# Performance work log

Hardware: AMD Instinct MI355X
Metric: run time of the kernel (lower is better)

## Reference

```python
import jax, jax.numpy as jnp
import numpy as np

B, S, D, H, E, K = 1, 2048, 1024, 16, 8, 2
DK = D // H          # 64 per-head key dim
FF = 4 * D           # 4096 expert hidden
EPS = 1e-5


def rmsnorm(x, scale):
    rms = jnp.sqrt(jnp.mean(x * x, axis=-1, keepdims=True) + EPS)
    return scale * (x / rms)


def setup_inputs() -> dict:
    key = jax.random.key(0)
    ks = jax.random.split(key, 12)
    std = 0.02
    x = jax.random.normal(ks[0], (B, S, D), dtype=jnp.float32)
    # causal mask: masked_fill where mask == 0
    self_attn_mask = jnp.tril(jnp.ones((S, S), dtype=jnp.int32))
    scale_attn = jnp.ones((D,), dtype=jnp.float32)
    scale_ffn = jnp.ones((D,), dtype=jnp.float32)
    # per-head projections, stacked: [H, DK, D] (torch Linear weight layout [out,in])
    Wq = jax.random.normal(ks[1], (H, DK, D), dtype=jnp.float32) * std
    Wk = jax.random.normal(ks[2], (H, DK, D), dtype=jnp.float32) * std
    Wv = jax.random.normal(ks[3], (H, DK, D), dtype=jnp.float32) * std
    Wo = jax.random.normal(ks[4], (D, D), dtype=jnp.float32) * std
    Wg = jax.random.normal(ks[5], (E, D), dtype=jnp.float32) * std   # router gate
    W_in = jax.random.normal(ks[6], (E, FF, D), dtype=jnp.float32) * std   # expert linear
    W_v = jax.random.normal(ks[7], (E, FF, D), dtype=jnp.float32) * std    # expert linear_v
    W_out = jax.random.normal(ks[8], (E, D, FF), dtype=jnp.float32) * std  # expert linear_out
    return {
        'x': x, 'self_attn_mask': self_attn_mask,
        'scale_attn': scale_attn, 'Wq': Wq, 'Wk': Wk, 'Wv': Wv, 'Wo': Wo,
        'scale_ffn': scale_ffn, 'Wg': Wg, 'W_in': W_in, 'W_v': W_v, 'W_out': W_out,
    }


def reference(x, self_attn_mask, scale_attn, Wq, Wk, Wv, Wo, scale_ffn, Wg, W_in, W_v, W_out):
    # --- self attention (pre-RMSNorm) ---
    normed = rmsnorm(x, scale_attn)
    q = jnp.einsum('bsd,hkd->bhsk', normed, Wq)
    k = jnp.einsum('bsd,hkd->bhsk', normed, Wk)
    v = jnp.einsum('bsd,hkd->bhsk', normed, Wv)
    attn = jnp.einsum('bhsk,bhtk->bhst', q, k) / np.sqrt(DK).astype(np.float32)
    attn = jnp.where(self_attn_mask[None, None] == 0, -jnp.inf, attn)
    attn = jax.nn.softmax(attn, axis=-1)
    ctx = jnp.einsum('bhst,bhtk->bhsk', attn, v)
    ctx = ctx.transpose(0, 2, 1, 3).reshape(x.shape[0], x.shape[1], D)  # concat heads
    a1 = ctx @ Wo.T
    x = x + a1
    # --- MoE (pre-RMSNorm) ---
    normed = rmsnorm(x, scale_ffn)
    router_logits = normed @ Wg.T                       # [B,S,E]
    router_probs = jax.nn.softmax(router_logits, axis=-1)
    gate, idx = jax.lax.top_k(router_probs, K)          # [B,S,K]
    gate = gate / jnp.sum(gate, axis=-1, keepdims=True)
    # combine weights per expert: sum of renormalized gates over selected slots
    onehot = (idx[..., None] == jnp.arange(E)).astype(x.dtype)  # [B,S,K,E]
    combine = jnp.sum(gate[..., None] * onehot, axis=2)         # [B,S,E]
    # all-expert dense FFN (faithful to the masked dense loop in torch)
    g = jax.nn.gelu(jnp.einsum('bsd,efd->bsef', normed, W_in), approximate=False)
    val = jnp.einsum('bsd,efd->bsef', normed, W_v)
    eo = jnp.einsum('bsef,edf->bsed', g * val, W_out)           # [B,S,E,D]
    moe_out = jnp.einsum('bse,bsed->bsd', combine, eo)
    out = x + moe_out
    return (out, router_probs)
```

## Files before the change

### kernel.cpp

```cpp
#include <hip/hip_runtime.h>
#include <hip/hip_bf16.h>
#include <math.h>

typedef unsigned int u32;
typedef unsigned short u16;
using bf16x8 = __attribute__((ext_vector_type(8))) short;
using f32x4 = __attribute__((ext_vector_type(4))) float;

#define MFMA_BF16(a, b, c) __builtin_amdgcn_mfma_f32_16x16x32_bf16((a), (b), (c), 0, 0, 0)
#define VMCNT8() asm volatile("s_waitcnt vmcnt(8)" ::: "memory")
#define VMCNT0() asm volatile("s_waitcnt vmcnt(0)" ::: "memory")
#define SBAR() __builtin_amdgcn_s_barrier()
#define SCHED0() __builtin_amdgcn_sched_barrier(0)

constexpr int kS = 2048, kD = 1024, kH = 16, kE = 8, kFF = 4096;
constexpr int kSlots = kS * 2;

__device__ __forceinline__ u16 bf16_rne(float f) {
  u32 u = __float_as_uint(f);
  u32 r = (u + 0x7fffu + ((u >> 16) & 1u)) >> 16;
  return (u16)r;
}
__device__ __forceinline__ float bf16_f32(u16 h) { return __uint_as_float(((u32)h) << 16); }
__device__ __forceinline__ u32 pack_hl(float x) {
  u16 hi = bf16_rne(x);
  u16 lo = bf16_rne(x - bf16_f32(hi));
  return ((u32)lo << 16) | (u32)hi;
}
__device__ __forceinline__ void unpack8(const u32* t, bf16x8& h, bf16x8& l) {
#pragma unroll
  for (int j = 0; j < 8; j++) {
    h[j] = (short)(t[j] & 0xffffu);
    l[j] = (short)(t[j] >> 16);
  }
}
__device__ __forceinline__ void gload_lds16(const void* g, void* l) {
  __builtin_amdgcn_global_load_lds((const __attribute__((address_space(1))) u32*)g,
                                   (__attribute__((address_space(3))) u32*)l, 16, 0, 0);
}

__global__ __launch_bounds__(256) void pack_dp3(const float* __restrict__ Wq,
                                                const float* __restrict__ Wk,
                                                const float* __restrict__ Wv,
                                                u16* __restrict__ o) {
  int i = blockIdx.x * 256 + threadIdx.x;
  if (i >= 3072 * 1024) return;
  int n = i >> 10, k = i & 1023;
  float v = (n < 1024) ? Wq[i] : (n < 2048) ? Wk[i - 1024 * 1024] : Wv[i - 2048 * 1024];
  u16 hi = bf16_rne(v);
  u16 lo = bf16_rne(v - bf16_f32(hi));
  size_t b = (size_t)n * 2048 + (size_t)(k >> 5) * 64 + (k & 31);
  o[b] = hi;
  o[b + 32] = lo;
}
__global__ __launch_bounds__(256) void pack_dp1(const float* __restrict__ W,
                                                u16* __restrict__ o, int n_elem) {
  int i = blockIdx.x * 256 + threadIdx.x;
  if (i >= n_elem) return;
  int k = i & 1023, n = i >> 10;
  float v = W[i];
  u16 hi = bf16_rne(v);
  u16 lo = bf16_rne(v - bf16_f32(hi));
  size_t b = (size_t)n * 2048 + (size_t)(k >> 5) * 64 + (k & 31);
  o[b] = hi;
  o[b + 32] = lo;
}
__global__ __launch_bounds__(256) void pack_bf16_kernel(const float* __restrict__ w,
                                                        u16* __restrict__ o, int n8) {
  int i = blockIdx.x * 256 + threadIdx.x;
  if (i >= n8) return;
  const float4* s = (const float4*)w + (size_t)i * 2;
  float4 a = s[0], b = s[1];
  u16 r[8] = {bf16_rne(a.x), bf16_rne(a.y), bf16_rne(a.z), bf16_rne(a.w),
              bf16_rne(b.x), bf16_rne(b.y), bf16_rne(b.z), bf16_rne(b.w)};
  *(uint4*)(o + (size_t)i * 8) = *(uint4*)r;
}

template <int MODE>
__global__ __launch_bounds__(256) void rmsnorm_kernel(
    const float* __restrict__ x, const float* __restrict__ scale,
    u16* __restrict__ odp, float* __restrict__ of32, u16* __restrict__ ob16) {
  const int s = blockIdx.x;
  const float* row = x + (size_t)s * kD;
  const int c = threadIdx.x * 4;
  float4 v = *(const float4*)(row + c);
  float ss = v.x * v.x + v.y * v.y + v.z * v.z + v.w * v.w;
#pragma unroll
  for (int m = 32; m; m >>= 1) ss += __shfl_xor(ss, m);
  __shared__ float wsum[4];
  if ((threadIdx.x & 63) == 0) wsum[threadIdx.x >> 6] = ss;
  __syncthreads();
  float tot = wsum[0] + wsum[1] + wsum[2] + wsum[3];
  float rinv = 1.0f / sqrtf(tot * (1.0f / kD) + 1e-5f);
  float4 sc = *(const float4*)(scale + c);
  float n[4] = {v.x * rinv * sc.x, v.y * rinv * sc.y, v.z * rinv * sc.z, v.w * rinv * sc.w};
  if (MODE == 0) {
    u16 hv[4], lv[4];
#pragma unroll
    for (int j = 0; j < 4; j++) {
      hv[j] = bf16_rne(n[j]);
      lv[j] = bf16_rne(n[j] - bf16_f32(hv[j]));
    }
    u16* o = odp + (size_t)s * 2048 + (size_t)(c >> 5) * 64 + (c & 31);
    *(uint2*)o = *(uint2*)hv;
    *(uint2*)(o + 32) = *(uint2*)lv;
  } else {
    *(float4*)(of32 + (size_t)s * kD + c) = make_float4(n[0], n[1], n[2], n[3]);
    u16* o = ob16 + (size_t)s * kD + c;
    o[0] = bf16_rne(n[0]); o[1] = bf16_rne(n[1]); o[2] = bf16_rne(n[2]); o[3] = bf16_rne(n[3]);
  }
}

template <int APK, int OUT>
__global__ __launch_bounds__(256) void gemm_dp(
    const void* __restrict__ Av, const u16* __restrict__ Bdp,
    const float* __restrict__ resid, int K,
    u32* __restrict__ oq, u32* __restrict__ ok, u32* __restrict__ ov,
    float* __restrict__ of) {
  __shared__ u16 As[2][128 * 64];
  __shared__ u16 Bs[2][128 * 64];
  const int tid = threadIdx.x, w = tid >> 6, l = tid & 63;
  const int m0 = blockIdx.y * 128, n0 = blockIdx.x * 128;
  const int wr = (w >> 1) * 64, wc = (w & 1) * 64;
  const char* Ab = (const char*)Av;
  const char* Bb = (const char*)Bdp;
  const size_t rowb = (size_t)K * 4;

  size_t asrc[4], bsrc[4];
  int dst[4];
#pragma unroll
  for (int i = 0; i < 4; i++) {
    int fl = i * 256 + tid;
    int row = fl >> 3, cb = fl & 7;
    size_t coff = (size_t)((cb ^ (row & 7)) * 16);
    asrc[i] = (size_t)(m0 + row) * rowb + coff;
    bsrc[i] = (size_t)(n0 + row) * rowb + coff;
    dst[i] = fl * 16;
  }

  f32x4 zero = {0.f, 0.f, 0.f, 0.f};
  f32x4 acc[4][4];
#pragma unroll
  for (int i = 0; i < 4; i++)
#pragma unroll
    for (int j = 0; j < 4; j++) acc[i][j] = zero;

  auto stage = [&](int buf, int s) {
    const char* ap = Ab + (size_t)s * 128;
    const char* bp = Bb + (size_t)s * 128;
#pragma unroll
    for (int i = 0; i < 4; i++) {
      gload_lds16(ap + asrc[i], (char*)&As[buf][0] + dst[i]);
      gload_lds16(bp + bsrc[i], (char*)&Bs[buf][0] + dst[i]);
    }
  };

  const int NS = K / 32;
  stage(0, 0);
  for (int s = 0; s < NS; s++) {
    const int cur = s & 1;
    const bool lastit = (s == NS - 1);
    if (!lastit) stage(cur ^ 1, s + 1);
    if (!lastit) VMCNT8(); else VMCNT0();
    SBAR();
    SCHED0();
    bf16x8 ah[4], al[4], bh[4], bl[4];
    const int g = l >> 4;
    if (APK) {
      const u32* At = (const u32*)&As[cur][0];
#pragma unroll
      for (int mi = 0; mi < 4; mi++) {
        int row = wr + mi * 16 + (l & 15);
        u32 t[8];
        *(uint4*)t = *(const uint4*)&At[row * 32 + (((2 * g) ^ (row & 7)) * 4)];
        *(uint4*)(t + 4) = *(const uint4*)&At[row * 32 + (((2 * g + 1) ^ (row & 7)) * 4)];
        unpack8(t, ah[mi], al[mi]);
      }
    } else {
#pragma unroll
      for (int mi = 0; mi < 4; mi++) {
        int row = wr + mi * 16 + (l & 15);
        ah[mi] = *(const bf16x8*)&As[cur][row * 64 + ((g ^ (row & 7)) * 8)];
        al[mi] = *(const bf16x8*)&As[cur][row * 64 + (((4 + g) ^ (row & 7)) * 8)];
      }
    }
#pragma unroll
    for (int ni = 0; ni < 4; ni++) {
      int row = wc + ni * 16 + (l & 15);
      bh[ni] = *(const bf16x8*)&Bs[cur][row * 64 + ((g ^ (row & 7)) * 8)];
      bl[ni] = *(const bf16x8*)&Bs[cur][row * 64 + (((4 + g) ^ (row & 7)) * 8)];
    }
#pragma unroll
    for (int mi = 0; mi < 4; mi++)
#pragma unroll
      for (int ni = 0; ni < 4; ni++) {
        f32x4 c = acc[mi][ni];
        c = MFMA_BF16(al[mi], bl[ni], c);
        c = MFMA_BF16(al[mi], bh[ni], c);
        c = MFMA_BF16(ah[mi], bl[ni], c);
        c = MFMA_BF16(ah[mi], bh[ni], c);
        acc[mi][ni] = c;
      }
    SCHED0();
    if (!lastit) SBAR();
  }

  if (OUT == 0) {
    u32* dstp;
    int nb;
    if (n0 < 1024) { dstp = oq; nb = n0; }
    else if (n0 < 2048) { dstp = ok; nb = n0 - 1024; }
    else { dstp = ov; nb = n0 - 2048; }
#pragma unroll
    for (int mi = 0; mi < 4; mi++)
#pragma unroll
      for (int ni = 0; ni < 4; ni++)
#pragma unroll
        for (int r = 0; r < 4; r++) {
          int row = m0 + wr + mi * 16 + ((l >> 4) << 2) + r;
          int col = nb + wc + ni * 16 + (l & 15);
          dstp[(size_t)row * 1024 + col] = pack_hl(acc[mi][ni][r]);
        }
  } else {
#pragma unroll
    for (int mi = 0; mi < 4; mi++)
#pragma unroll
      for (int ni = 0; ni < 4; ni++)
#pragma unroll
        for (int r = 0; r < 4; r++) {
          int row = m0 + wr + mi * 16 + ((l >> 4) << 2) + r;
          int col = n0 + wc + ni * 16 + (l & 15);
          of[(size_t)row * 1024 + col] = resid[(size_t)row * 1024 + col] + acc[mi][ni][r];
        }
  }
}

__global__ __launch_bounds__(256) void attn_kernel(
    const u32* __restrict__ Qp, const u32* __restrict__ Kp, const u32* __restrict__ Vp,
    u32* __restrict__ Op) {
  constexpr int LDK = 68;
  __shared__ u32 Ks[64 * LDK];
  __shared__ u32 Vs[64 * LDK];
  __shared__ u32 Ps[64 * LDK];
  const int tid = threadIdx.x, w = tid >> 6, l = tid & 63;
  const int qt = blockIdx.x, hh = blockIdx.y;
  const int q0 = qt * 64, hc = hh * 64;

  bf16x8 qh[2], ql[2];
  {
    const int qrow = q0 + w * 16 + (l & 15);
#pragma unroll
    for (int kk = 0; kk < 2; kk++) {
      u32 t[8];
      const u32* p = Qp + (size_t)qrow * kD + hc + kk * 32 + ((l >> 4) << 3);
      *(uint4*)t = *(const uint4*)p;
      *(uint4*)(t + 4) = *(const uint4*)(p + 4);
      unpack8(t, qh[kk], ql[kk]);
    }
  }
  float mrun[4], lrun[4];
  f32x4 zero = {0.f, 0.f, 0.f, 0.f};
  f32x4 oacc[4];
#pragma unroll
  for (int r = 0; r < 4; r++) { mrun[r] = -3.0e38f; lrun[r] = 0.f; }
#pragma unroll
  for (int vb = 0; vb < 4; vb++) oacc[vb] = zero;

  for (int kt = 0; kt <= qt; kt++) {
    __syncthreads();
    {
      const int trow = tid >> 2, c0 = (tid & 3) * 16;
      const u32* gK = Kp + (size_t)(kt * 64 + trow) * kD + hc + c0;
      u32* sK = Ks + trow * LDK + c0;
      *(uint4*)sK = *(const uint4*)gK;
      *(uint4*)(sK + 4) = *(const uint4*)(gK + 4);
      *(uint4*)(sK + 8) = *(const uint4*)(gK + 8);
      *(uint4*)(sK + 12) = *(const uint4*)(gK + 12);
      const u32* gV = Vp + (size_t)(kt * 64 + trow) * kD + hc + c0;
#pragma unroll
      for (int j = 0; j < 16; j += 4) {
        uint4 v = *(const uint4*)(gV + j);
        Vs[(c0 + j + 0) * LDK + trow] = v.x;
        Vs[(c0 + j + 1) * LDK + trow] = v.y;
        Vs[(c0 + j + 2) * LDK + trow] = v.z;
        Vs[(c0 + j + 3) * LDK + trow] = v.w;
      }
    }
    __syncthreads();

    f32x4 sfr[4];
#pragma unroll
    for (int kb = 0; kb < 4; kb++) {
      f32x4 sa = zero;
#pragma unroll
      for (int kk = 0; kk < 2; kk++) {
        u32 t[8];
        bf16x8 kh, kl;
        const u32* p = Ks + (kb * 16 + (l & 15)) * LDK + kk * 32 + ((l >> 4) << 3);
        *(uint4*)t = *(const uint4*)p;
        *(uint4*)(t + 4) = *(const uint4*)(p + 4);
        unpack8(t, kh, kl);
        sa = MFMA_BF16(ql[kk], kl, sa);
        sa = MFMA_BF16(ql[kk], kh, sa);
        sa = MFMA_BF16(qh[kk], kl, sa);
        sa = MFMA_BF16(qh[kk], kh, sa);
      }
      sfr[kb] = sa * 0.125f;
    }
    if (kt == qt) {
#pragma unroll
      for (int kb = 0; kb < 4; kb++) {
        int t = kt * 64 + kb * 16 + (l & 15);
#pragma unroll
        for (int r = 0; r < 4; r++) {
          int qq = q0 + w * 16 + ((l >> 4) << 2) + r;
          if (t > qq) sfr[kb][r] = -3.0e38f;
        }
      }
    }
#pragma unroll
    for (int r = 0; r < 4; r++) {
      float mx = fmaxf(fmaxf(sfr[0][r], sfr[1][r]), fmaxf(sfr[2][r], sfr[3][r]));
#pragma unroll
      for (int mm = 1; mm < 16; mm <<= 1) mx = fmaxf(mx, __shfl_xor(mx, mm));
      float mnew = fmaxf(mrun[r], mx);
      float sf = __expf(mrun[r] - mnew);
      mrun[r] = mnew;
      float rs = 0.f;
#pragma unroll
      for (int kb = 0; kb < 4; kb++) {
        float p = __expf(sfr[kb][r] - mnew);
        sfr[kb][r] = p;
        rs += p;
      }
#pragma unroll
      for (int mm = 1; mm < 16; mm <<= 1) rs += __shfl_xor(rs, mm);
      lrun[r] = lrun[r] * sf + rs;
#pragma unroll
      for (int vb = 0; vb < 4; vb++) oacc[vb][r] *= sf;
    }
#pragma unroll
    for (int kb = 0; kb < 4; kb++)
#pragma unroll
      for (int r = 0; r < 4; r++)
        Ps[(w * 16 + ((l >> 4) << 2) + r) * LDK + kb * 16 + (l & 15)] = pack_hl(sfr[kb][r]);
#pragma unroll
    for (int ks = 0; ks < 2; ks++) {
      bf16x8 ph, pl;
      {
        u32 t[8];
        const u32* pp = Ps + (w * 16 + (l & 15)) * LDK + ks * 32 + ((l >> 4) << 3);
        *(uint4*)t = *(const uint4*)pp;
        *(uint4*)(t + 4) = *(const uint4*)(pp + 4);
        unpack8(t, ph, pl);
      }
#pragma unroll
      for (int vb = 0; vb < 4; vb++) {
        u32 t2[8];
        bf16x8 vh, vl;
        const u32* pv = Vs + (vb * 16 + (l & 15)) * LDK + ks * 32 + ((l >> 4) << 3);
        *(uint4*)t2 = *(const uint4*)pv;
        *(uint4*)(t2 + 4) = *(const uint4*)(pv + 4);
        unpack8(t2, vh, vl);
        f32x4 c = oacc[vb];
        c = MFMA_BF16(pl, vl, c);
        c = MFMA_BF16(pl, vh, c);
        c = MFMA_BF16(ph, vl, c);
        c = MFMA_BF16(ph, vh, c);
        oacc[vb] = c;
      }
    }
  }
#pragma unroll
  for (int vb = 0; vb < 4; vb++)
#pragma unroll
    for (int r = 0; r < 4; r++) {
      float o = oacc[vb][r] / lrun[r];
      int row = q0 + w * 16 + ((l >> 4) << 2) + r;
      int col = hc + vb * 16 + (l & 15);
      Op[(size_t)row * kD + col] = pack_hl(o);
    }
}

__global__ __launch_bounds__(256) void router_kernel(
    const float* __restrict__ normed, const float* __restrict__ Wg,
    float* __restrict__ probs, float* __restrict__ gates,
    int* __restrict__ experts, int* __restrict__ counts) {
  const int w = threadIdx.x >> 6, l = threadIdx.x & 63;
  const int s = blockIdx.x * 4 + w;
  float lg[kE];
  const float* row = normed + (size_t)s * kD;
#pragma unroll
  for (int e = 0; e < kE; e++) {
    const float* wg = Wg + (size_t)e * kD;
    float a = 0.f;
    for (int d = l; d < kD; d += 64) a += row[d] * wg[d];
#pragma unroll
    for (int m = 32; m; m >>= 1) a += __shfl_xor(a, m);
    lg[e] = a;
  }
  if (l == 0) {
    float mx = lg[0];
#pragma unroll
    for (int e = 1; e < kE; e++) mx = fmaxf(mx, lg[e]);
    float p[kE], sum = 0.f;
#pragma unroll
    for (int e = 0; e < kE; e++) { p[e] = __expf(lg[e] - mx); sum += p[e]; }
    float inv = 1.f / sum;
#pragma unroll
    for (int e = 0; e < kE; e++) { p[e] *= inv; probs[(size_t)s * kE + e] = p[e]; }
    int i1 = 0;
#pragma unroll
    for (int e = 1; e < kE; e++) if (lg[e] > lg[i1]) i1 = e;
    int i2 = (i1 == 0) ? 1 : 0;
#pragma unroll
    for (int e = 0; e < kE; e++) if (e != i1 && lg[e] > lg[i2]) i2 = e;
    float den = 1.f / (p[i1] + p[i2]);
    gates[s * 2] = p[i1] * den;
    gates[s * 2 + 1] = p[i2] * den;
    experts[s * 2] = i1;
    experts[s * 2 + 1] = i2;
    atomicAdd(&counts[i1], 1);
    atomicAdd(&counts[i2], 1);
  }
}

__global__ void moe_init(int* counts) {
  if (threadIdx.x < kE) counts[threadIdx.x] = 0;
}
__global__ void moe_scan(const int* __restrict__ counts, int* __restrict__ ebase,
                         int* __restrict__ cursor) {
  if (threadIdx.x == 0) {
    int acc = 0;
    for (int e = 0; e < kE; e++) { ebase[e] = acc; cursor[e] = acc; acc += counts[e]; }
    ebase[kE] = acc;
  }
}
__global__ void moe_fill(const int* __restrict__ experts, int* __restrict__ cursor,
                         int* __restrict__ slot_list, int* __restrict__ slot_of) {
  int s = blockIdx.x * 256 + threadIdx.x;
  if (s >= kS) return;
  for (int k = 0; k < 2; k++) {
    int e = experts[s * 2 + k];
    int pos = atomicAdd(&cursor[e], 1);
    slot_list[pos] = s;
    slot_of[s * 2 + k] = pos;
  }
}

__global__ __launch_bounds__(512) void moe_mm1(
    const u16* __restrict__ A, const u16* __restrict__ B1g, const u16* __restrict__ B2g,
    const int* __restrict__ slot_list, const int* __restrict__ ebase,
    u16* __restrict__ Uo) {
  const int e = blockIdx.z;
  const int base = ebase[e];
  const int Me = ebase[e + 1] - base;
  const int m0 = blockIdx.y * 256;
  if (m0 >= Me) return;
  const int n0 = blockIdx.x * 128;
  __shared__ u16 As[2][256 * 64];
  __shared__ u16 B1s[2][128 * 64];
  __shared__ u16 B2s[2][128 * 64];
  const int tid = threadIdx.x, w = tid >> 6, l = tid & 63;
  const int wr = (w >> 2) * 128, wc = (w & 3) * 32;
  const char* B1 = (const char*)(B1g + (size_t)e * kFF * kD);
  const char* B2 = (const char*)(B2g + (size_t)e * kFF * kD);

  size_t asrc[4], bsrc[2];
  int adst[4], bdst[2];
#pragma unroll
  for (int i = 0; i < 4; i++) {
    int fl = i * 512 + tid;
    int row = fl >> 3, cb = fl & 7;
    int mr = m0 + row;
    if (mr > Me - 1) mr = Me - 1;
    int ar = slot_list[base + mr];
    asrc[i] = (size_t)ar * 2048 + (size_t)((cb ^ (row & 7)) * 16);
    adst[i] = fl * 16;
  }
#pragma unroll
  for (int i = 0; i < 2; i++) {
    int fl = i * 512 + tid;
    int row = fl >> 3, cb = fl & 7;
    bsrc[i] = (size_t)(n0 + row) * 2048 + (size_t)((cb ^ (row & 7)) * 16);
    bdst[i] = fl * 16;
  }

  f32x4 zero = {0.f, 0.f, 0.f, 0.f};
  f32x4 acc1[8][2], acc2[8][2];
#pragma unroll
  for (int i = 0; i < 8; i++)
#pragma unroll
    for (int j = 0; j < 2; j++) { acc1[i][j] = zero; acc2[i][j] = zero; }

  auto stage = [&](int buf, int s) {
    const size_t so = (size_t)s * 128;
    const char* ab = (const char*)A + so;
#pragma unroll
    for (int i = 0; i < 4; i++) gload_lds16(ab + asrc[i], (char*)&As[buf][0] + adst[i]);
#pragma unroll
    for (int i = 0; i < 2; i++) {
      gload_lds16(B1 + so + bsrc[i], (char*)&B1s[buf][0] + bdst[i]);
      gload_lds16(B2 + so + bsrc[i], (char*)&B2s[buf][0] + bdst[i]);
    }
  };

  const int NS = kD / 64;
  stage(0, 0);
  for (int s = 0; s < NS; s++) {
    const int cur = s & 1;
    const bool lastit = (s == NS - 1);
    if (!lastit) stage(cur ^ 1, s + 1);
    if (!lastit) VMCNT8(); else VMCNT0();
    SBAR();
    SCHED0();
#pragma unroll
    for (int kk = 0; kk < 2; kk++) {
      const int g = kk * 4 + (l >> 4);
      bf16x8 af[8], b1f[2], b2f[2];
#pragma unroll
      for (int mi = 0; mi < 8; mi++) {
        int row = wr + mi * 16 + (l & 15);
        af[mi] = *(const bf16x8*)&As[cur][row * 64 + ((g ^ (row & 7)) * 8)];
      }
#pragma unroll
      for (int ni = 0; ni < 2; ni++) {
        int row = wc + ni * 16 + (l & 15);
        int bo = row * 64 + ((g ^ (row & 7)) * 8);
        b1f[ni] = *(const bf16x8*)&B1s[cur][bo];
        b2f[ni] = *(const bf16x8*)&B2s[cur][bo];
      }
#pragma unroll
      for (int mi = 0; mi < 8; mi++)
#pragma unroll
        for (int ni = 0; ni < 2; ni++) {
          acc1[mi][ni] = MFMA_BF16(af[mi], b1f[ni], acc1[mi][ni]);
          acc2[mi][ni] = MFMA_BF16(af[mi], b2f[ni], acc2[mi][ni]);
        }
    }
    SCHED0();
    if (!lastit) SBAR();
  }

#pragma unroll
  for (int mi = 0; mi < 8; mi++)
#pragma unroll
    for (int r = 0; r < 4; r++) {
      int ml = m0 + wr + mi * 16 + ((l >> 4) << 2) + r;
      if (ml >= Me) continue;
      size_t rb = (size_t)(base + ml) * kFF;
#pragma unroll
      for (int ni = 0; ni < 2; ni++) {
        int col = n0 + wc + ni * 16 + (l & 15);
        float u = acc1[mi][ni][r], v2 = acc2[mi][ni][r];
        float ge = 0.5f * u * (1.0f + erff(u * 0.70710678118654752f));
        Uo[rb + col] = bf16_rne(ge * v2);
      }
    }
}

__global__ __launch_bounds__(256) void moe_mm2(
    const u16* __restrict__ U, const u16* __restrict__ Bg,
    const int* __restrict__ ebase, float* __restrict__ eo) {
  const int e = blockIdx.z;
  const int base = ebase[e];
  const int Me = ebase[e + 1] - base;
  const int m0 = blockIdx.y * 128;
  if (m0 >= Me) return;
  const int n0 = blockIdx.x * 128;
  __shared__ u16 As[2][128 * 64];
  __shared__ u16 Bs[2][128 * 64];
  const int tid = threadIdx.x, w = tid >> 6, l = tid & 63;
  const int wr = (w >> 1) * 64, wc = (w & 1) * 64;
  const char* B = (const char*)(Bg + (size_t)e * kD * kFF);

  size_t asrc[4], bsrc[4];
  int dst[4];
#pragma unroll
  for (int i = 0; i < 4; i++) {
    int fl = i * 256 + tid;
    int row = fl >> 3, cb = fl & 7;
    size_t coff = (size_t)((cb ^ (row & 7)) * 16);
    int mr = m0 + row;
    if (mr > Me - 1) mr = Me - 1;
    asrc[i] = (size_t)(base + mr) * 8192 + coff;
    bsrc[i] = (size_t)(n0 + row) * 8192 + coff;
    dst[i] = fl * 16;
  }

  f32x4 zero = {0.f, 0.f, 0.f, 0.f};
  f32x4 acc[4][4];
#pragma unroll
  for (int i = 0; i < 4; i++)
#pragma unroll
    for (int j = 0; j < 4; j++) acc[i][j] = zero;

  auto stage = [&](int buf, int s) {
    const size_t so = (size_t)s * 128;
#pragma unroll
    for (int i = 0; i < 4; i++) {
      gload_lds16((const char*)U + so + asrc[i], (char*)&As[buf][0] + dst[i]);
      gload_lds16(B + so + bsrc[i], (char*)&Bs[buf][0] + dst[i]);
    }
  };

  const int NS = kFF / 64;
  stage(0, 0);
  for (int s = 0; s < NS; s++) {
    const int cur = s & 1;
    const bool lastit = (s == NS - 1);
    if (!lastit) stage(cur ^ 1, s + 1);
    if (!lastit) VMCNT8(); else VMCNT0();
    SBAR();
    SCHED0();
#pragma unroll
    for (int kk = 0; kk < 2; kk++) {
      const int g = kk * 4 + (l >> 4);
      bf16x8 af[4], bf[4];
#pragma unroll
      for (int mi = 0; mi < 4; mi++) {
        int row = wr + mi * 16 + (l & 15);
        af[mi] = *(const bf16x8*)&As[cur][row * 64 + ((g ^ (row & 7)) * 8)];
      }
#pragma unroll
      for (int ni = 0; ni < 4; ni++) {
        int row = wc + ni * 16 + (l & 15);
        bf[ni] = *(const bf16x8*)&Bs[cur][row * 64 + ((g ^ (row & 7)) * 8)];
      }
#pragma unroll
      for (int mi = 0; mi < 4; mi++)
#pragma unroll
        for (int ni = 0; ni < 4; ni++) acc[mi][ni] = MFMA_BF16(af[mi], bf[ni], acc[mi][ni]);
    }
    SCHED0();
    if (!lastit) SBAR();
  }

#pragma unroll
  for (int mi = 0; mi < 4; mi++)
#pragma unroll
    for (int r = 0; r < 4; r++) {
      int ml = m0 + wr + mi * 16 + ((l >> 4) << 2) + r;
      if (ml >= Me) continue;
      size_t rb = (size_t)(base + ml) * kD;
#pragma unroll
      for (int ni = 0; ni < 4; ni++) {
        int col = n0 + wc + ni * 16 + (l & 15);
        eo[rb + col] = acc[mi][ni][r];
      }
    }
}

__global__ __launch_bounds__(256) void combine_kernel(
    const float* __restrict__ h, const float* __restrict__ eo,
    const float* __restrict__ gates, const int* __restrict__ slot_of,
    float* __restrict__ out) {
  const int s = blockIdx.x;
  const float g0 = gates[s * 2], g1 = gates[s * 2 + 1];
  const int p0 = slot_of[s * 2], p1 = slot_of[s * 2 + 1];
  const int c = threadIdx.x * 4;
  float4 hv = *(const float4*)(h + (size_t)s * kD + c);
  float4 e0 = *(const float4*)(eo + (size_t)p0 * kD + c);
  float4 e1 = *(const float4*)(eo + (size_t)p1 * kD + c);
  float4 o;
  o.x = hv.x + g0 * e0.x + g1 * e1.x;
  o.y = hv.y + g0 * e0.y + g1 * e1.y;
  o.z = hv.z + g0 * e0.z + g1 * e1.z;
  o.w = hv.w + g0 * e0.w + g1 * e1.w;
  *(float4*)(out + (size_t)s * kD + c) = o;
}

extern "C" void kernel_launch(void* const* d_in, const int* in_sizes, int n_in,
                              void* d_out, int out_size, void* d_ws, size_t ws_size,
                              hipStream_t stream) {
  (void)in_sizes; (void)n_in; (void)out_size; (void)ws_size;
  const float* x = (const float*)d_in[0];
  const float* scale_attn = (const float*)d_in[2];
  const float* Wq = (const float*)d_in[3];
  const float* Wk = (const float*)d_in[4];
  const float* Wv = (const float*)d_in[5];
  const float* Wo = (const float*)d_in[6];
  const float* scale_ffn = (const float*)d_in[7];
  const float* Wg = (const float*)d_in[8];
  const float* W_in = (const float*)d_in[9];
  const float* W_vv = (const float*)d_in[10];
  const float* W_out = (const float*)d_in[11];
  float* out = (float*)d_out;
  float* probs = out + (size_t)kS * kD;

  char* wsb = (char*)d_ws;
  size_t off = 0;
  auto alloc = [&](size_t bytes) -> void* {
    void* p = wsb + off;
    off += (bytes + 255) & ~(size_t)255;
    return p;
  };
  const size_t SDu = (size_t)kS * kD;
  const size_t EW = (size_t)kE * kFF * kD;
  u16* normA_dp = (u16*)alloc(SDu * 2 * 2);
  u32* qpk = (u32*)alloc(SDu * 4);
  u32* kpk = (u32*)alloc(SDu * 4);
  u32* vpk = (u32*)alloc(SDu * 4);
  u32* ctxpk = (u32*)alloc(SDu * 4);
  float* h = (float*)alloc(SDu * 4);
  float* normFf = (float*)alloc(SDu * 4);
  u16* normFb = (u16*)alloc(SDu * 2);
  u16* Wqkv_dp = (u16*)alloc((size_t)3072 * 2048 * 2);
  u16* Wo_dp = (u16*)alloc((size_t)1024 * 2048 * 2);
  u16* Win_bf = (u16*)alloc(EW * 2);
  u16* Wv_bf = (u16*)alloc(EW * 2);
  u16* Wout_bf = (u16*)alloc(EW * 2);
  u16* U = (u16*)alloc((size_t)kSlots * kFF * 2);
  float* eo = (float*)alloc((size_t)kSlots * kD * 4);
  float* gates = (float*)alloc(kS * 2 * 4);
  int* experts = (int*)alloc(kS * 2 * 4);
  int* slot_of = (int*)alloc(kS * 2 * 4);
  int* slot_list = (int*)alloc(kSlots * 4);
  int* counts = (int*)alloc(64);
  int* ebase = (int*)alloc(64);
  int* cursor = (int*)alloc(64);

  pack_dp3<<<(3072 * 1024) / 256, 256, 0, stream>>>(Wq, Wk, Wv, Wqkv_dp);
  pack_dp1<<<(1024 * 1024) / 256, 256, 0, stream>>>(Wo, Wo_dp, 1024 * 1024);
  const int n8 = (int)(EW / 8);
  pack_bf16_kernel<<<(n8 + 255) / 256, 256, 0, stream>>>(W_in, Win_bf, n8);
  pack_bf16_kernel<<<(n8 + 255) / 256, 256, 0, stream>>>(W_vv, Wv_bf, n8);
  pack_bf16_kernel<<<(n8 + 255) / 256, 256, 0, stream>>>(W_out, Wout_bf, n8);

  rmsnorm_kernel<0><<<kS, 256, 0, stream>>>(x, scale_attn, normA_dp, nullptr, nullptr);
  gemm_dp<0, 0><<<dim3(3072 / 128, kS / 128), 256, 0, stream>>>(
      normA_dp, Wqkv_dp, nullptr, kD, qpk, kpk, vpk, nullptr);
  attn_kernel<<<dim3(kS / 64, kH), 256, 0, stream>>>(qpk, kpk, vpk, ctxpk);
  gemm_dp<1, 1><<<dim3(1024 / 128, kS / 128), 256, 0, stream>>>(
      ctxpk, Wo_dp, x, kD, nullptr, nullptr, nullptr, h);

  rmsnorm_kernel<1><<<kS, 256, 0, stream>>>(h, scale_ffn, nullptr, normFf, normFb);
  moe_init<<<1, 64, 0, stream>>>(counts);
  router_kernel<<<kS / 4, 256, 0, stream>>>(normFf, Wg, probs, gates, experts, counts);
  moe_scan<<<1, 64, 0, stream>>>(counts, ebase, cursor);
  moe_fill<<<kS / 256, 256, 0, stream>>>(experts, cursor, slot_list, slot_of);

  moe_mm1<<<dim3(kFF / 128, kSlots / 256, kE), 512, 0, stream>>>(
      normFb, Win_bf, Wv_bf, slot_list, ebase, U);
  moe_mm2<<<dim3(kD / 128, kSlots / 128, kE), 256, 0, stream>>>(
      U, Wout_bf, ebase, eo);

  combine_kernel<<<kS, 256, 0, stream>>>(h, eo, gates, slot_of, out);
}
```

Measured before the change: 699.2 us.

## Use compacted tile map for MoE GEMMs, split GELU, prefetch attention K/V

The MoE GEMMs now launch over a compacted list of 128-row tiles built in moe_scan, so no blocks are spent on empty per-expert grid slots. W_in and W_v are packed into one concatenated matrix and computed by a single GEMM; a separate gelu_mul kernel then applies GELU and the gate product. moe_mm2 narrows its N tile to 64. The attention kernel register-prefetches the next K/V tile while the current one is computed. This adds a kernel launch and an extra round trip of the raw Uraw intermediate through memory, and Uraw is placed at the start of the workspace, where it aliases other buffers.

```diff
diff --git a/kernel.cpp b/kernel.cpp
--- a/kernel.cpp
+++ b/kernel.cpp
@@ -9,12 +9,14 @@
 
 #define MFMA_BF16(a, b, c) __builtin_amdgcn_mfma_f32_16x16x32_bf16((a), (b), (c), 0, 0, 0)
 #define VMCNT8() asm volatile("s_waitcnt vmcnt(8)" ::: "memory")
+#define VMCNT6() asm volatile("s_waitcnt vmcnt(6)" ::: "memory")
 #define VMCNT0() asm volatile("s_waitcnt vmcnt(0)" ::: "memory")
 #define SBAR() __builtin_amdgcn_s_barrier()
 #define SCHED0() __builtin_amdgcn_sched_barrier(0)
 
 constexpr int kS = 2048, kD = 1024, kH = 16, kE = 8, kFF = 4096;
-constexpr int kSlots = kS * 2;
+constexpr int kSlotCap = 5120;
+constexpr int kMaxTiles = 40;
 
 __device__ __forceinline__ u16 bf16_rne(float f) {
   u32 u = __float_as_uint(f);
@@ -64,6 +66,23 @@
   size_t b = (size_t)n * 2048 + (size_t)(k >> 5) * 64 + (k & 31);
   o[b] = hi;
   o[b + 32] = lo;
+}
+__global__ __launch_bounds__(256) void pack_winv(const float* __restrict__ Wi,
+                                                 const float* __restrict__ Wv,
+                                                 u16* __restrict__ o) {
+  size_t i8 = (size_t)blockIdx.x * 256 + threadIdx.x;
+  if (i8 >= (size_t)kE * 8192 * 1024 / 8) return;
+  size_t flat = i8 * 8;
+  int e = (int)(flat >> 23);
+  int r = (int)(flat & ((1u << 23) - 1));
+  int n = r >> 10, k = r & 1023;
+  const float* src = (n < 4096) ? Wi + ((size_t)e * 4096 + n) * 1024 + k
+                                : Wv + ((size_t)e * 4096 + (n - 4096)) * 1024 + k;
+  float4 a = *(const float4*)src;
+  float4 b = *(const float4*)(src + 4);
+  u16 rr[8] = {bf16_rne(a.x), bf16_rne(a.y), bf16_rne(a.z), bf16_rne(a.w),
+               bf16_rne(b.x), bf16_rne(b.y), bf16_rne(b.z), bf16_rne(b.w)};
+  *(uint4*)(o + flat) = *(uint4*)rr;
 }
 __global__ __launch_bounds__(256) void pack_bf16_kernel(const float* __restrict__ w,
                                                         u16* __restrict__ o, int n8) {
@@ -266,27 +285,41 @@
 #pragma unroll
   for (int vb = 0; vb < 4; vb++) oacc[vb] = zero;
 
+  const int trow = tid >> 2, c0v = (tid & 3) * 16;
+  const u32* gKb = Kp + hc + c0v;
+  const u32* gVb = Vp + hc + c0v;
+  uint4 kr[4], vr[4];
+  {
+    const u32* gK = gKb + (size_t)trow * kD;
+    kr[0] = *(const uint4*)gK; kr[1] = *(const uint4*)(gK + 4);
+    kr[2] = *(const uint4*)(gK + 8); kr[3] = *(const uint4*)(gK + 12);
+    const u32* gV = gVb + (size_t)trow * kD;
+    vr[0] = *(const uint4*)gV; vr[1] = *(const uint4*)(gV + 4);
+    vr[2] = *(const uint4*)(gV + 8); vr[3] = *(const uint4*)(gV + 12);
+  }
+
   for (int kt = 0; kt <= qt; kt++) {
+    {
+      u32* sK = Ks + trow * LDK + c0v;
+      *(uint4*)sK = kr[0]; *(uint4*)(sK + 4) = kr[1];
+      *(uint4*)(sK + 8) = kr[2]; *(uint4*)(sK + 12) = kr[3];
+#pragma unroll
+      for (int j = 0; j < 4; j++) {
+        Vs[(c0v + j * 4 + 0) * LDK + trow] = vr[j].x;
+        Vs[(c0v + j * 4 + 1) * LDK + trow] = vr[j].y;
+        Vs[(c0v + j * 4 + 2) * LDK + trow] = vr[j].z;
+        Vs[(c0v + j * 4 + 3) * LDK + trow] = vr[j].w;
+      }
+    }
     __syncthreads();
-    {
-      const int trow = tid >> 2, c0 = (tid & 3) * 16;
-      const u32* gK = Kp + (size_t)(kt * 64 + trow) * kD + hc + c0;
-      u32* sK = Ks + trow * LDK + c0;
-      *(uint4*)sK = *(const uint4*)gK;
-      *(uint4*)(sK + 4) = *(const uint4*)(gK + 4);
-      *(uint4*)(sK + 8) = *(const uint4*)(gK + 8);
-      *(uint4*)(sK + 12) = *(const uint4*)(gK + 12);
-      const u32* gV = Vp + (size_t)(kt * 64 + trow) * kD + hc + c0;
-#pragma unroll
-      for (int j = 0; j < 16; j += 4) {
-        uint4 v = *(const uint4*)(gV + j);
-        Vs[(c0 + j + 0) * LDK + trow] = v.x;
-        Vs[(c0 + j + 1) * LDK + trow] = v.y;
-        Vs[(c0 + j + 2) * LDK + trow] = v.z;
-        Vs[(c0 + j + 3) * LDK + trow] = v.w;
-      }
-    }
-    __syncthreads();
+    if (kt < qt) {
+      const u32* gK = gKb + (size_t)((kt + 1) * 64 + trow) * kD;
+      kr[0] = *(const uint4*)gK; kr[1] = *(const uint4*)(gK + 4);
+      kr[2] = *(const uint4*)(gK + 8); kr[3] = *(const uint4*)(gK + 12);
+      const u32* gV = gVb + (size_t)((kt + 1) * 64 + trow) * kD;
+      vr[0] = *(const uint4*)gV; vr[1] = *(const uint4*)(gV + 4);
+      vr[2] = *(const uint4*)(gV + 8); vr[3] = *(const uint4*)(gV + 12);
+    }
 
     f32x4 sfr[4];
 #pragma unroll
@@ -370,6 +403,7 @@
         oacc[vb] = c;
       }
     }
+    __syncthreads();
   }
 #pragma unroll
   for (int vb = 0; vb < 4; vb++)
@@ -429,11 +463,18 @@
   if (threadIdx.x < kE) counts[threadIdx.x] = 0;
 }
 __global__ void moe_scan(const int* __restrict__ counts, int* __restrict__ ebase,
-                         int* __restrict__ cursor) {
+                         int* __restrict__ cursor, int2* __restrict__ tmap) {
   if (threadIdx.x == 0) {
-    int acc = 0;
-    for (int e = 0; e < kE; e++) { ebase[e] = acc; cursor[e] = acc; acc += counts[e]; }
+    int acc = 0, t = 0;
+    for (int e = 0; e < kE; e++) {
+      ebase[e] = acc;
+      cursor[e] = acc;
+      int nt = (counts[e] + 127) >> 7;
+      for (int i = 0; i < nt; i++) tmap[t++] = make_int2(e, i * 128);
+      acc += nt << 7;
+    }
     ebase[kE] = acc;
+    for (; t < kMaxTiles; t++) tmap[t] = make_int2(-1, 0);
   }
 }
 __global__ void moe_fill(const int* __restrict__ experts, int* __restrict__ cursor,
@@ -448,60 +489,51 @@
   }
 }
 
-__global__ __launch_bounds__(512) void moe_mm1(
-    const u16* __restrict__ A, const u16* __restrict__ B1g, const u16* __restrict__ B2g,
-    const int* __restrict__ slot_list, const int* __restrict__ ebase,
-    u16* __restrict__ Uo) {
-  const int e = blockIdx.z;
-  const int base = ebase[e];
-  const int Me = ebase[e + 1] - base;
-  const int m0 = blockIdx.y * 256;
-  if (m0 >= Me) return;
+__global__ __launch_bounds__(256) void moe_mmA(
+    const u16* __restrict__ A, const u16* __restrict__ Bg,
+    const int* __restrict__ slot_list, const int* __restrict__ counts,
+    const int* __restrict__ ebase, const int2* __restrict__ tmap,
+    u16* __restrict__ Uraw) {
+  int2 tm = tmap[blockIdx.y];
+  const int e = tm.x;
+  if (e < 0) return;
+  const int base = ebase[e], Me = counts[e], m0 = tm.y;
   const int n0 = blockIdx.x * 128;
-  __shared__ u16 As[2][256 * 64];
-  __shared__ u16 B1s[2][128 * 64];
-  __shared__ u16 B2s[2][128 * 64];
+  __shared__ u16 As[2][128 * 64];
+  __shared__ u16 Bs[2][128 * 64];
   const int tid = threadIdx.x, w = tid >> 6, l = tid & 63;
-  const int wr = (w >> 2) * 128, wc = (w & 3) * 32;
-  const char* B1 = (const char*)(B1g + (size_t)e * kFF * kD);
-  const char* B2 = (const char*)(B2g + (size_t)e * kFF * kD);
-
-  size_t asrc[4], bsrc[2];
-  int adst[4], bdst[2];
+  const int wr = (w >> 1) * 64, wc = (w & 1) * 64;
+  const char* Ab = (const char*)A;
+  const char* Bb = (const char*)(Bg + ((size_t)e * 8192) * 1024);
+
+  size_t asrc[4], bsrc[4];
+  int dst[4];
 #pragma unroll
   for (int i = 0; i < 4; i++) {
-    int fl = i * 512 + tid;
+    int fl = i * 256 + tid;
     int row = fl >> 3, cb = fl & 7;
+    size_t coff = (size_t)((cb ^ (row & 7)) * 16);
     int mr = m0 + row;
     if (mr > Me - 1) mr = Me - 1;
     int ar = slot_list[base + mr];
-    asrc[i] = (size_t)ar * 2048 + (size_t)((cb ^ (row & 7)) * 16);
-    adst[i] = fl * 16;
-  }
-#pragma unroll
-  for (int i = 0; i < 2; i++) {
-    int fl = i * 512 + tid;
-    int row = fl >> 3, cb = fl & 7;
-    bsrc[i] = (size_t)(n0 + row) * 2048 + (size_t)((cb ^ (row & 7)) * 16);
-    bdst[i] = fl * 16;
+    asrc[i] = (size_t)ar * 2048 + coff;
+    bsrc[i] = (size_t)(n0 + row) * 2048 + coff;
+    dst[i] = fl * 16;
   }
 
   f32x4 zero = {0.f, 0.f, 0.f, 0.f};
-  f32x4 acc1[8][2], acc2[8][2];
-#pragma unroll
-  for (int i = 0; i < 8; i++)
-#pragma unroll
-    for (int j = 0; j < 2; j++) { acc1[i][j] = zero; acc2[i][j] = zero; }
+  f32x4 acc[4][4];
+#pragma unroll
+  for (int i = 0; i < 4; i++)
+#pragma unroll
+    for (int j = 0; j < 4; j++) acc[i][j] = zero;
 
   auto stage = [&](int buf, int s) {
     const size_t so = (size_t)s * 128;
-    const char* ab = (const char*)A + so;
-#pragma unroll
-    for (int i = 0; i < 4; i++) gload_lds16(ab + asrc[i], (char*)&As[buf][0] + adst[i]);
-#pragma unroll
-    for (int i = 0; i < 2; i++) {
-      gload_lds16(B1 + so + bsrc[i], (char*)&B1s[buf][0] + bdst[i]);
-      gload_lds16(B2 + so + bsrc[i], (char*)&B2s[buf][0] + bdst[i]);
+#pragma unroll
+    for (int i = 0; i < 4; i++) {
+      gload_lds16(Ab + so + asrc[i], (char*)&As[buf][0] + dst[i]);
+      gload_lds16(Bb + so + bsrc[i], (char*)&Bs[buf][0] + dst[i]);
     }
   };
 
@@ -517,91 +549,110 @@
 #pragma unroll
     for (int kk = 0; kk < 2; kk++) {
       const int g = kk * 4 + (l >> 4);
-      bf16x8 af[8], b1f[2], b2f[2];
-#pragma unroll
-      for (int mi = 0; mi < 8; mi++) {
+      bf16x8 af[4], bfr[4];
+#pragma unroll
+      for (int mi = 0; mi < 4; mi++) {
         int row = wr + mi * 16 + (l & 15);
         af[mi] = *(const bf16x8*)&As[cur][row * 64 + ((g ^ (row & 7)) * 8)];
       }
 #pragma unroll
-      for (int ni = 0; ni < 2; ni++) {
+      for (int ni = 0; ni < 4; ni++) {
         int row = wc + ni * 16 + (l & 15);
-        int bo = row * 64 + ((g ^ (row & 7)) * 8);
-        b1f[ni] = *(const bf16x8*)&B1s[cur][bo];
-        b2f[ni] = *(const bf16x8*)&B2s[cur][bo];
-      }
-#pragma unroll
-      for (int mi = 0; mi < 8; mi++)
-#pragma unroll
-        for (int ni = 0; ni < 2; ni++) {
-          acc1[mi][ni] = MFMA_BF16(af[mi], b1f[ni], acc1[mi][ni]);
-          acc2[mi][ni] = MFMA_BF16(af[mi], b2f[ni], acc2[mi][ni]);
-        }
+        bfr[ni] = *(const bf16x8*)&Bs[cur][row * 64 + ((g ^ (row & 7)) * 8)];
+      }
+#pragma unroll
+      for (int mi = 0; mi < 4; mi++)
+#pragma unroll
+        for (int ni = 0; ni < 4; ni++) acc[mi][ni] = MFMA_BF16(af[mi], bfr[ni], acc[mi][ni]);
     }
     SCHED0();
     if (!lastit) SBAR();
   }
 
 #pragma unroll
-  for (int mi = 0; mi < 8; mi++)
+  for (int mi = 0; mi < 4; mi++)
 #pragma unroll
     for (int r = 0; r < 4; r++) {
       int ml = m0 + wr + mi * 16 + ((l >> 4) << 2) + r;
       if (ml >= Me) continue;
-      size_t rb = (size_t)(base + ml) * kFF;
-#pragma unroll
-      for (int ni = 0; ni < 2; ni++) {
+      size_t rb = (size_t)(base + ml) * 8192;
+#pragma unroll
+      for (int ni = 0; ni < 4; ni++) {
         int col = n0 + wc + ni * 16 + (l & 15);
-        float u = acc1[mi][ni][r], v2 = acc2[mi][ni][r];
-        float ge = 0.5f * u * (1.0f + erff(u * 0.70710678118654752f));
-        Uo[rb + col] = bf16_rne(ge * v2);
-      }
-    }
+        Uraw[rb + col] = bf16_rne(acc[mi][ni][r]);
+      }
+    }
+}
+
+__global__ __launch_bounds__(256) void gelu_mul(const u16* __restrict__ Uraw,
+                                                u16* __restrict__ H) {
+  size_t i8 = (size_t)blockIdx.x * 256 + threadIdx.x;
+  if (i8 >= (size_t)kSlotCap * kFF / 8) return;
+  int row = (int)(i8 >> 9);
+  int j8 = ((int)i8 & 511) * 8;
+  const u16* up = Uraw + (size_t)row * 8192 + j8;
+  uint4 uu = *(const uint4*)up;
+  uint4 vv = *(const uint4*)(up + 4096);
+  const u16* ue = (const u16*)&uu;
+  const u16* ve = (const u16*)&vv;
+  u16 o[8];
+#pragma unroll
+  for (int k = 0; k < 8; k++) {
+    float u = bf16_f32(ue[k]), v = bf16_f32(ve[k]);
+    float ge = 0.5f * u * (1.0f + erff(u * 0.70710678118654752f));
+    o[k] = bf16_rne(ge * v);
+  }
+  *(uint4*)(H + (size_t)row * kFF + j8) = *(uint4*)o;
 }
 
 __global__ __launch_bounds__(256) void moe_mm2(
-    const u16* __restrict__ U, const u16* __restrict__ Bg,
-    const int* __restrict__ ebase, float* __restrict__ eo) {
-  const int e = blockIdx.z;
-  const int base = ebase[e];
-  const int Me = ebase[e + 1] - base;
-  const int m0 = blockIdx.y * 128;
-  if (m0 >= Me) return;
-  const int n0 = blockIdx.x * 128;
+    const u16* __restrict__ H, const u16* __restrict__ Bg,
+    const int* __restrict__ counts, const int* __restrict__ ebase,
+    const int2* __restrict__ tmap, float* __restrict__ eo) {
+  int2 tm = tmap[blockIdx.y];
+  const int e = tm.x;
+  if (e < 0) return;
+  const int base = ebase[e], Me = counts[e], m0 = tm.y;
+  const int n0 = blockIdx.x * 64;
   __shared__ u16 As[2][128 * 64];
-  __shared__ u16 Bs[2][128 * 64];
+  __shared__ u16 Bs[2][64 * 64];
   const int tid = threadIdx.x, w = tid >> 6, l = tid & 63;
-  const int wr = (w >> 1) * 64, wc = (w & 1) * 64;
-  const char* B = (const char*)(Bg + (size_t)e * kD * kFF);
-
-  size_t asrc[4], bsrc[4];
-  int dst[4];
+  const int wr = (w >> 1) * 64, wc = (w & 1) * 32;
+  const char* Ab = (const char*)H;
+  const char* Bb = (const char*)(Bg + (size_t)e * kD * kFF);
+
+  size_t asrc[4], bsrc[2];
+  int adst[4], bdst[2];
 #pragma unroll
   for (int i = 0; i < 4; i++) {
     int fl = i * 256 + tid;
     int row = fl >> 3, cb = fl & 7;
-    size_t coff = (size_t)((cb ^ (row & 7)) * 16);
     int mr = m0 + row;
     if (mr > Me - 1) mr = Me - 1;
-    asrc[i] = (size_t)(base + mr) * 8192 + coff;
-    bsrc[i] = (size_t)(n0 + row) * 8192 + coff;
-    dst[i] = fl * 16;
+    asrc[i] = (size_t)(base + mr) * 8192 + (size_t)((cb ^ (row & 7)) * 16);
+    adst[i] = fl * 16;
+  }
+#pragma unroll
+  for (int i = 0; i < 2; i++) {
+    int fl = i * 256 + tid;
+    int row = fl >> 3, cb = fl & 7;
+    bsrc[i] = (size_t)(n0 + row) * 8192 + (size_t)((cb ^ (row & 7)) * 16);
+    bdst[i] = fl * 16;
   }
 
   f32x4 zero = {0.f, 0.f, 0.f, 0.f};
-  f32x4 acc[4][4];
+  f32x4 acc[4][2];
 #pragma unroll
   for (int i = 0; i < 4; i++)
 #pragma unroll
-    for (int j = 0; j < 4; j++) acc[i][j] = zero;
+    for (int j = 0; j < 2; j++) acc[i][j] = zero;
 
   auto stage = [&](int buf, int s) {
     const size_t so = (size_t)s * 128;
 #pragma unroll
-    for (int i = 0; i < 4; i++) {
-      gload_lds16((const char*)U + so + asrc[i], (char*)&As[buf][0] + dst[i]);
-      gload_lds16(B + so + bsrc[i], (char*)&Bs[buf][0] + dst[i]);
-    }
+    for (int i = 0; i < 4; i++) gload_lds16(Ab + so + asrc[i], (char*)&As[buf][0] + adst[i]);
+#pragma unroll
+    for (int i = 0; i < 2; i++) gload_lds16(Bb + so + bsrc[i], (char*)&Bs[buf][0] + bdst[i]);
   };
 
   const int NS = kFF / 64;
@@ -610,27 +661,27 @@
     const int cur = s & 1;
     const bool lastit = (s == NS - 1);
     if (!lastit) stage(cur ^ 1, s + 1);
-    if (!lastit) VMCNT8(); else VMCNT0();
+    if (!lastit) VMCNT6(); else VMCNT0();
     SBAR();
     SCHED0();
 #pragma unroll
     for (int kk = 0; kk < 2; kk++) {
       const int g = kk * 4 + (l >> 4);
-      bf16x8 af[4], bf[4];
+      bf16x8 af[4], bfr[2];
 #pragma unroll
       for (int mi = 0; mi < 4; mi++) {
         int row = wr + mi * 16 + (l & 15);
         af[mi] = *(const bf16x8*)&As[cur][row * 64 + ((g ^ (row & 7)) * 8)];
       }
 #pragma unroll
-      for (int ni = 0; ni < 4; ni++) {
+      for (int ni = 0; ni < 2; ni++) {
         int row = wc + ni * 16 + (l & 15);
-        bf[ni] = *(const bf16x8*)&Bs[cur][row * 64 + ((g ^ (row & 7)) * 8)];
+        bfr[ni] = *(const bf16x8*)&Bs[cur][row * 64 + ((g ^ (row & 7)) * 8)];
       }
 #pragma unroll
       for (int mi = 0; mi < 4; mi++)
 #pragma unroll
-        for (int ni = 0; ni < 4; ni++) acc[mi][ni] = MFMA_BF16(af[mi], bf[ni], acc[mi][ni]);
+        for (int ni = 0; ni < 2; ni++) acc[mi][ni] = MFMA_BF16(af[mi], bfr[ni], acc[mi][ni]);
     }
     SCHED0();
     if (!lastit) SBAR();
@@ -644,7 +695,7 @@
       if (ml >= Me) continue;
       size_t rb = (size_t)(base + ml) * kD;
 #pragma unroll
-      for (int ni = 0; ni < 4; ni++) {
+      for (int ni = 0; ni < 2; ni++) {
         int col = n0 + wc + ni * 16 + (l & 15);
         eo[rb + col] = acc[mi][ni][r];
       }
@@ -696,36 +747,35 @@
     return p;
   };
   const size_t SDu = (size_t)kS * kD;
-  const size_t EW = (size_t)kE * kFF * kD;
-  u16* normA_dp = (u16*)alloc(SDu * 2 * 2);
+  u16* Uraw = (u16*)wsb;
+  u16* normA_dp = (u16*)alloc(SDu * 4);
   u32* qpk = (u32*)alloc(SDu * 4);
   u32* kpk = (u32*)alloc(SDu * 4);
   u32* vpk = (u32*)alloc(SDu * 4);
   u32* ctxpk = (u32*)alloc(SDu * 4);
-  float* h = (float*)alloc(SDu * 4);
-  float* normFf = (float*)alloc(SDu * 4);
-  u16* normFb = (u16*)alloc(SDu * 2);
   u16* Wqkv_dp = (u16*)alloc((size_t)3072 * 2048 * 2);
   u16* Wo_dp = (u16*)alloc((size_t)1024 * 2048 * 2);
-  u16* Win_bf = (u16*)alloc(EW * 2);
-  u16* Wv_bf = (u16*)alloc(EW * 2);
-  u16* Wout_bf = (u16*)alloc(EW * 2);
-  u16* U = (u16*)alloc((size_t)kSlots * kFF * 2);
-  float* eo = (float*)alloc((size_t)kSlots * kD * 4);
+  float* normFf = (float*)alloc(SDu * 4);
+  float* eo = (float*)alloc((size_t)kSlotCap * kD * 4);
+  float* h = (float*)alloc(SDu * 4);
+  u16* normFb = (u16*)alloc(SDu * 2);
+  u16* Winv_bf = (u16*)alloc((size_t)kE * 8192 * 1024 * 2);
+  u16* Wout_bf = (u16*)alloc((size_t)kE * kD * kFF * 2);
+  u16* H = (u16*)alloc((size_t)kSlotCap * kFF * 2);
   float* gates = (float*)alloc(kS * 2 * 4);
   int* experts = (int*)alloc(kS * 2 * 4);
   int* slot_of = (int*)alloc(kS * 2 * 4);
-  int* slot_list = (int*)alloc(kSlots * 4);
+  int* slot_list = (int*)alloc(kSlotCap * 4);
   int* counts = (int*)alloc(64);
   int* ebase = (int*)alloc(64);
   int* cursor = (int*)alloc(64);
+  int2* tmap = (int2*)alloc(kMaxTiles * 8);
 
   pack_dp3<<<(3072 * 1024) / 256, 256, 0, stream>>>(Wq, Wk, Wv, Wqkv_dp);
   pack_dp1<<<(1024 * 1024) / 256, 256, 0, stream>>>(Wo, Wo_dp, 1024 * 1024);
-  const int n8 = (int)(EW / 8);
-  pack_bf16_kernel<<<(n8 + 255) / 256, 256, 0, stream>>>(W_in, Win_bf, n8);
-  pack_bf16_kernel<<<(n8 + 255) / 256, 256, 0, stream>>>(W_vv, Wv_bf, n8);
-  pack_bf16_kernel<<<(n8 + 255) / 256, 256, 0, stream>>>(W_out, Wout_bf, n8);
+  pack_winv<<<(int)((size_t)kE * 8192 * 1024 / 8 / 256), 256, 0, stream>>>(W_in, W_vv, Winv_bf);
+  const int n8o = (int)((size_t)kE * kD * kFF / 8);
+  pack_bf16_kernel<<<(n8o + 255) / 256, 256, 0, stream>>>(W_out, Wout_bf, n8o);
 
   rmsnorm_kernel<0><<<kS, 256, 0, stream>>>(x, scale_attn, normA_dp, nullptr, nullptr);
   gemm_dp<0, 0><<<dim3(3072 / 128, kS / 128), 256, 0, stream>>>(
@@ -737,13 +787,14 @@
   rmsnorm_kernel<1><<<kS, 256, 0, stream>>>(h, scale_ffn, nullptr, normFf, normFb);
   moe_init<<<1, 64, 0, stream>>>(counts);
   router_kernel<<<kS / 4, 256, 0, stream>>>(normFf, Wg, probs, gates, experts, counts);
-  moe_scan<<<1, 64, 0, stream>>>(counts, ebase, cursor);
+  moe_scan<<<1, 64, 0, stream>>>(counts, ebase, cursor, tmap);
   moe_fill<<<kS / 256, 256, 0, stream>>>(experts, cursor, slot_list, slot_of);
 
-  moe_mm1<<<dim3(kFF / 128, kSlots / 256, kE), 512, 0, stream>>>(
-      normFb, Win_bf, Wv_bf, slot_list, ebase, U);
-  moe_mm2<<<dim3(kD / 128, kSlots / 128, kE), 256, 0, stream>>>(
-      U, Wout_bf, ebase, eo);
+  moe_mmA<<<dim3(8192 / 128, kMaxTiles), 256, 0, stream>>>(
+      normFb, Winv_bf, slot_list, counts, ebase, tmap, Uraw);
+  gelu_mul<<<(int)((size_t)kSlotCap * kFF / 8 / 256), 256, 0, stream>>>(Uraw, H);
+  moe_mm2<<<dim3(kD / 64, kMaxTiles), 256, 0, stream>>>(
+      H, Wout_bf, counts, ebase, tmap, eo);
 
   combine_kernel<<<kS, 256, 0, stream>>>(h, eo, gates, slot_of, out);
 }
```

After: 719.6 us. 1.03x slower.
